# Optimization experiments

Hardware: AMD Instinct MI355X
Metric: run time of the kernel (lower is better)

The kernel has to match this reference:

```python
import jax, jax.numpy as jnp
import numpy as np

N_SEGMENTS = 16384

def setup_inputs() -> dict:
    key = jax.random.key(0)
    k1, k2, k3, k4 = jax.random.split(key, 4)
    N, D = 500000, 128
    x = jax.random.normal(k1, (N, D), dtype=jnp.float32)
    index = jnp.sort(jax.random.randint(k2, (N,), 0, N_SEGMENTS, dtype=jnp.int64))
    Wg = jax.random.normal(k3, (D, 1), dtype=jnp.float32) * 0.05
    bg = jnp.zeros((1,), dtype=jnp.float32)
    Wm = jax.random.normal(k4, (D, D), dtype=jnp.float32) * 0.05
    bm = jnp.zeros((D,), dtype=jnp.float32)
    return {"x": x, "index": index, "Wg": Wg, "bg": bg, "Wm": Wm, "bm": bm}

def reference(x, index, Wg, bg, Wm, bm):
    # gate_nn: Linear(d, 1)
    gate = x @ Wg + bg  # [N, 1]
    # segment softmax over nodes grouped by index (numerically stable)
    seg_max = jax.ops.segment_max(gate, index, num_segments=N_SEGMENTS)  # [S, 1]
    gate = jnp.exp(gate - seg_max[index])
    denom = jax.ops.segment_sum(gate, index, num_segments=N_SEGMENTS)[index] + 1e-10
    gate = gate / denom  # [N, 1]
    # message_nn: Linear(d, d)
    m = x @ Wm + bm  # [N, D]
    # weighted segment reduce
    out = jax.ops.segment_sum(gate * m, index, num_segments=N_SEGMENTS)  # [S, D]
    return out
```

## Files before the change

kernel.cpp:

```cpp
#include <hip/hip_runtime.h>

#define D 128

__global__ void init_kernel(int* __restrict__ segstart, int* __restrict__ segend,
                            unsigned* __restrict__ flag, int S) {
    int i = blockIdx.x * blockDim.x + threadIdx.x;
    if (i < S) { segstart[i] = 0; segend[i] = 0; }
    if (i == 0) *flag = 0u;
}

__global__ void detect_kernel(const unsigned* __restrict__ words, int half,
                              unsigned* __restrict__ flag) {
    unsigned v = 0;
    int stride = gridDim.x * blockDim.x;
    for (int n = blockIdx.x * blockDim.x + threadIdx.x; n < half; n += stride)
        v |= words[2 * n + 1];
#pragma unroll
    for (int m = 32; m; m >>= 1) v |= __shfl_xor(v, m, 64);
    if ((threadIdx.x & 63) == 0 && v) atomicOr(flag, 1u);
}

__device__ __forceinline__ int idx_at(const int* __restrict__ w, int n, bool is64) {
    return is64 ? w[2 * n] : w[n];
}

__global__ void bounds_kernel(const int* __restrict__ w, const unsigned* __restrict__ flag,
                              int N, int* __restrict__ segstart, int* __restrict__ segend) {
    int n = blockIdx.x * blockDim.x + threadIdx.x;
    if (n >= N) return;
    bool is64 = (*flag == 0u);
    int i = idx_at(w, n, is64);
    if (n == 0 || idx_at(w, n - 1, is64) != i) segstart[i] = n;
    if (n == N - 1 || idx_at(w, n + 1, is64) != i) segend[i] = n + 1;
}

__global__ __launch_bounds__(256) void seg_attn_kernel(
    const float* __restrict__ x, const int* __restrict__ segstart,
    const int* __restrict__ segend, const float* __restrict__ Wg,
    const float* __restrict__ bg, float* __restrict__ wx,
    float* __restrict__ segf, int S) {
    const int wid = threadIdx.x >> 6;
    const int lane = threadIdx.x & 63;
    const int s = blockIdx.x * 4 + wid;
    if (s >= S) return;
    const int start = segstart[s];
    const int end = segend[s];
    const int half = lane >> 5;
    const int c4 = (lane & 31) * 4;
    const float4 wg4 = *(const float4*)&Wg[c4];
    const float b0 = bg[0];
    float4 acc = {0.f, 0.f, 0.f, 0.f};
    float usum = 0.f;
    int r = start;
    for (; r + 8 <= end; r += 8) {
        const float4 a0 = *(const float4*)&x[(size_t)(r + 0 + half) * D + c4];
        const float4 a1 = *(const float4*)&x[(size_t)(r + 2 + half) * D + c4];
        const float4 a2 = *(const float4*)&x[(size_t)(r + 4 + half) * D + c4];
        const float4 a3 = *(const float4*)&x[(size_t)(r + 6 + half) * D + c4];
        float p0 = a0.x * wg4.x + a0.y * wg4.y + a0.z * wg4.z + a0.w * wg4.w;
        float p1 = a1.x * wg4.x + a1.y * wg4.y + a1.z * wg4.z + a1.w * wg4.w;
        float p2 = a2.x * wg4.x + a2.y * wg4.y + a2.z * wg4.z + a2.w * wg4.w;
        float p3 = a3.x * wg4.x + a3.y * wg4.y + a3.z * wg4.z + a3.w * wg4.w;
#pragma unroll
        for (int m = 1; m <= 16; m <<= 1) {
            p0 += __shfl_xor(p0, m, 64);
            p1 += __shfl_xor(p1, m, 64);
            p2 += __shfl_xor(p2, m, 64);
            p3 += __shfl_xor(p3, m, 64);
        }
        const float e0 = __expf(p0 + b0);
        const float e1 = __expf(p1 + b0);
        const float e2 = __expf(p2 + b0);
        const float e3 = __expf(p3 + b0);
        usum += (e0 + e1) + (e2 + e3);
        acc.x += e0 * a0.x + e1 * a1.x + e2 * a2.x + e3 * a3.x;
        acc.y += e0 * a0.y + e1 * a1.y + e2 * a2.y + e3 * a3.y;
        acc.z += e0 * a0.z + e1 * a1.z + e2 * a2.z + e3 * a3.z;
        acc.w += e0 * a0.w + e1 * a1.w + e2 * a2.w + e3 * a3.w;
    }
    for (; r < end; r += 2) {
        int row = r + half;
        if (row > end - 1) row = end - 1;
        const float4 a = *(const float4*)&x[(size_t)row * D + c4];
        float p = a.x * wg4.x + a.y * wg4.y + a.z * wg4.z + a.w * wg4.w;
#pragma unroll
        for (int m = 1; m <= 16; m <<= 1) p += __shfl_xor(p, m, 64);
        float e = __expf(p + b0);
        if (half && r + 1 >= end) e = 0.f;
        usum += e;
        acc.x += e * a.x;
        acc.y += e * a.y;
        acc.z += e * a.z;
        acc.w += e * a.w;
    }
    usum += __shfl_xor(usum, 32, 64);
    acc.x += __shfl_xor(acc.x, 32, 64);
    acc.y += __shfl_xor(acc.y, 32, 64);
    acc.z += __shfl_xor(acc.z, 32, 64);
    acc.w += __shfl_xor(acc.w, 32, 64);
    const float inv = 1.f / (usum + 1e-10f);
    if (half == 0) {
        float4 o;
        o.x = acc.x * inv;
        o.y = acc.y * inv;
        o.z = acc.z * inv;
        o.w = acc.w * inv;
        *(float4*)&wx[(size_t)s * D + c4] = o;
    }
    if (lane == 0) segf[s] = usum * inv;
}

__global__ __launch_bounds__(64) void gemm_kernel(
    float* __restrict__ out, const float* __restrict__ Wm,
    const float* __restrict__ bm, const float* __restrict__ segf) {
    __shared__ float tile[16 * 128];
    const int s0 = blockIdx.x * 16;
    const int tid = threadIdx.x;
    for (int t = tid; t < 16 * 128; t += 64) tile[t] = out[(size_t)s0 * 128 + t];
    __syncthreads();
    float2 acc[16];
#pragma unroll
    for (int r = 0; r < 16; ++r) { acc[r].x = 0.f; acc[r].y = 0.f; }
    for (int k = 0; k < 128; ++k) {
        const float2 wm = *(const float2*)&Wm[k * 128 + 2 * tid];
#pragma unroll
        for (int r = 0; r < 16; ++r) {
            const float wv = tile[r * 128 + k];
            acc[r].x += wv * wm.x;
            acc[r].y += wv * wm.y;
        }
    }
    const float2 bmv = *(const float2*)&bm[2 * tid];
#pragma unroll
    for (int r = 0; r < 16; ++r) {
        const int s = s0 + r;
        const float f = segf[s];
        float2 o;
        o.x = acc[r].x + f * bmv.x;
        o.y = acc[r].y + f * bmv.y;
        *(float2*)&out[(size_t)s * 128 + 2 * tid] = o;
    }
}

extern "C" void kernel_launch(void* const* d_in, const int* in_sizes, int n_in,
                              void* d_out, int out_size, void* d_ws, size_t ws_size,
                              hipStream_t stream) {
    const float* x  = (const float*)d_in[0];
    const int*   w  = (const int*)d_in[1];
    const float* Wg = (const float*)d_in[2];
    const float* bg = (const float*)d_in[3];
    const float* Wm = (const float*)d_in[4];
    const float* bm = (const float*)d_in[5];
    float* out = (float*)d_out;

    const int N = in_sizes[1];
    const int S = out_size / D;

    char* wsb = (char*)d_ws;
    unsigned* flag = (unsigned*)wsb;
    int* segstart = (int*)(wsb + 256);
    int* segend = segstart + S;
    float* segf = (float*)(segend + S);

    init_kernel<<<(S + 255) / 256, 256, 0, stream>>>(segstart, segend, flag, S);
    detect_kernel<<<256, 256, 0, stream>>>((const unsigned*)w, N / 2, flag);
    bounds_kernel<<<(N + 255) / 256, 256, 0, stream>>>(w, flag, N, segstart, segend);
    seg_attn_kernel<<<(S + 3) / 4, 256, 0, stream>>>(x, segstart, segend, Wg, bg,
                                                     out, segf, S);
    gemm_kernel<<<S / 16, 64, 0, stream>>>(out, Wm, bm, segf);
}
```

Baseline: 409.0 us.

## Compute segment offsets by binary search and drop init/detect kernels

```diff
diff --git a/kernel.cpp b/kernel.cpp
--- a/kernel.cpp
+++ b/kernel.cpp
@@ -1,50 +1,41 @@
 #include <hip/hip_runtime.h>
 
 #define D 128
-
-__global__ void init_kernel(int* __restrict__ segstart, int* __restrict__ segend,
-                            unsigned* __restrict__ flag, int S) {
-    int i = blockIdx.x * blockDim.x + threadIdx.x;
-    if (i < S) { segstart[i] = 0; segend[i] = 0; }
-    if (i == 0) *flag = 0u;
-}
-
-__global__ void detect_kernel(const unsigned* __restrict__ words, int half,
-                              unsigned* __restrict__ flag) {
-    unsigned v = 0;
-    int stride = gridDim.x * blockDim.x;
-    for (int n = blockIdx.x * blockDim.x + threadIdx.x; n < half; n += stride)
-        v |= words[2 * n + 1];
-#pragma unroll
-    for (int m = 32; m; m >>= 1) v |= __shfl_xor(v, m, 64);
-    if ((threadIdx.x & 63) == 0 && v) atomicOr(flag, 1u);
-}
 
 __device__ __forceinline__ int idx_at(const int* __restrict__ w, int n, bool is64) {
     return is64 ? w[2 * n] : w[n];
 }
 
-__global__ void bounds_kernel(const int* __restrict__ w, const unsigned* __restrict__ flag,
-                              int N, int* __restrict__ segstart, int* __restrict__ segend) {
-    int n = blockIdx.x * blockDim.x + threadIdx.x;
-    if (n >= N) return;
-    bool is64 = (*flag == 0u);
-    int i = idx_at(w, n, is64);
-    if (n == 0 || idx_at(w, n - 1, is64) != i) segstart[i] = n;
-    if (n == N - 1 || idx_at(w, n + 1, is64) != i) segend[i] = n + 1;
+__global__ __launch_bounds__(256) void bounds_kernel(
+    const int* __restrict__ w, int N, int S, int* __restrict__ segstart) {
+    const int lane = threadIdx.x & 63;
+    const int quarter = N >> 2;
+    const int n0 = quarter + (int)(((long long)(quarter - 64) * lane) / 64);
+    unsigned v = ((const unsigned*)w)[2 * n0 + 1];
+#pragma unroll
+    for (int m = 32; m; m >>= 1) v |= __shfl_xor(v, m, 64);
+    const bool is64 = (v == 0u);
+    const int s = blockIdx.x * blockDim.x + threadIdx.x;
+    if (s > S) return;
+    if (s == S) { segstart[S] = N; return; }
+    int lo = 0, hi = N;
+    while (lo < hi) {
+        const int mid = (lo + hi) >> 1;
+        if (idx_at(w, mid, is64) < s) lo = mid + 1; else hi = mid;
+    }
+    segstart[s] = lo;
 }
 
 __global__ __launch_bounds__(256) void seg_attn_kernel(
     const float* __restrict__ x, const int* __restrict__ segstart,
-    const int* __restrict__ segend, const float* __restrict__ Wg,
-    const float* __restrict__ bg, float* __restrict__ wx,
-    float* __restrict__ segf, int S) {
+    const float* __restrict__ Wg, const float* __restrict__ bg,
+    float* __restrict__ wx, float* __restrict__ segf, int S) {
     const int wid = threadIdx.x >> 6;
     const int lane = threadIdx.x & 63;
     const int s = blockIdx.x * 4 + wid;
     if (s >= S) return;
     const int start = segstart[s];
-    const int end = segend[s];
+    const int end = segstart[s + 1];
     const int half = lane >> 5;
     const int c4 = (lane & 31) * 4;
     const float4 wg4 = *(const float4*)&Wg[c4];
@@ -157,15 +148,11 @@
     const int S = out_size / D;
 
     char* wsb = (char*)d_ws;
-    unsigned* flag = (unsigned*)wsb;
-    int* segstart = (int*)(wsb + 256);
-    int* segend = segstart + S;
-    float* segf = (float*)(segend + S);
+    int* segstart = (int*)wsb;
+    float* segf = (float*)(segstart + S + 1);
 
-    init_kernel<<<(S + 255) / 256, 256, 0, stream>>>(segstart, segend, flag, S);
-    detect_kernel<<<256, 256, 0, stream>>>((const unsigned*)w, N / 2, flag);
-    bounds_kernel<<<(N + 255) / 256, 256, 0, stream>>>(w, flag, N, segstart, segend);
-    seg_attn_kernel<<<(S + 3) / 4, 256, 0, stream>>>(x, segstart, segend, Wg, bg,
+    bounds_kernel<<<(S + 1 + 255) / 256, 256, 0, stream>>>(w, N, S, segstart);
+    seg_attn_kernel<<<(S + 3) / 4, 256, 0, stream>>>(x, segstart, Wg, bg,
                                                      out, segf, S);
     gemm_kernel<<<S / 16, 64, 0, stream>>>(out, Wm, bm, segf);
 }
```

After: 399.0 us. 1.02x faster.
